# Kernel tuning notes

Measured on AMD Instinct MI355X. Metric: run time of the kernel, lower is better.

## Reference

```python
import jax, jax.numpy as jnp
import numpy as np

E = 16   # n_experts
K = 4    # top_k
NEG = jnp.float32(-1e20)


def _swiglu(x, w1, w2, w3):
    # bias-free SwiGLU expert: (swish(x@w1) * (x@w2)) @ w3
    a = x @ w1
    return (a * jax.nn.sigmoid(a) * (x @ w2)) @ w3


def setup_inputs() -> dict:
    key = jax.random.key(0)
    ks = jax.random.split(key, 9)
    B, S, D, H = 32, 512, 512, 1365  # H = D*2*4//3
    s = 0.02  # weight init scale to keep activations sane
    return {
        "x": jax.random.normal(ks[0], (B, S, D), jnp.float32),
        "gate_w": jax.random.normal(ks[1], (D, E), jnp.float32) * s,
        "routing_bias": jnp.zeros((E,), jnp.float32),
        "w1": jax.random.normal(ks[2], (E, D, H), jnp.float32) * s,
        "w2": jax.random.normal(ks[3], (E, D, H), jnp.float32) * s,
        "w3": jax.random.normal(ks[4], (E, H, D), jnp.float32) * s,
        "sw1": jax.random.normal(ks[5], (D, H), jnp.float32) * s,
        "sw2": jax.random.normal(ks[6], (D, H), jnp.float32) * s,
        "sw3": jax.random.normal(ks[7], (H, D), jnp.float32) * s,
    }


def reference(x, gate_w, routing_bias, w1, w2, w3, sw1, sw2, sw3):
    # gate logits + aux-free load-balancing bias  [B,S,E]
    gate_out = x @ gate_w + routing_bias
    top_v, top_i = jax.lax.top_k(gate_out, K)
    # chosen[b,s,e] = 1 if expert e is in the top-k for token (b,s)
    chosen = jax.nn.one_hot(top_i, E, dtype=x.dtype).sum(axis=-2)
    # scatter top-k values onto a -1e20 background, then softmax over experts
    masked = jnp.where(chosen > 0, gate_out, NEG)
    probs = jax.nn.softmax(masked, axis=-1)
    weights = probs * chosen  # zero outside the chosen set (matches torch mask)
    # shared expert runs on all tokens
    out = _swiglu(x, sw1, sw2, sw3)
    # per-expert SwiGLU, weighted-combined (loop over fixed small E)
    for e in range(E):
        out = out + _swiglu(x, w1[e], w2[e], w3[e]) * weights[..., e:e + 1]
    return out
```

## Files before the change

### kernel.cpp

```cpp
#include <hip/hip_runtime.h>

#define NT    16384
#define DDIM  512
#define HDIM  1365
#define HPAD  1408
#define NEXP  16
#define BK    64
#define BM    128
#define MAXTILES 656
#define MAXSLOTS 83968

typedef unsigned short u16;
typedef unsigned int   u32;
typedef __attribute__((ext_vector_type(8))) __bf16 bf16x8;
typedef __attribute__((ext_vector_type(4))) float  f32x4;
typedef __attribute__((address_space(3))) void lds_void;
typedef __attribute__((address_space(1))) void glb_void;

__device__ __forceinline__ u16 f2bf(float f) {
  union { float f; u32 u; } v; v.f = f;
  u32 u = v.u;
  u += 0x7fffu + ((u >> 16) & 1u);
  return (u16)(u >> 16);
}

__device__ __forceinline__ float bf2f(u16 b) {
  union { u32 u; float f; } v; v.u = ((u32)b) << 16;
  return v.f;
}

__device__ __forceinline__ f32x4 mfma16(bf16x8 a, bf16x8 b, f32x4 c) {
  return __builtin_amdgcn_mfma_f32_16x16x32_bf16(a, b, c, 0, 0, 0);
}

__device__ __forceinline__ void gload16(const u16* g, u16* l) {
  __builtin_amdgcn_global_load_lds((const glb_void*)g, (lds_void*)l, 16, 0, 0);
}

__device__ __forceinline__ bf16x8 lds_frag(const u16* base, int row, int e0) {
  int b = ((row << 7) + (e0 << 1)) ^ ((row & 7) << 4);
  return *(const bf16x8*)((const char*)base + b);
}

__device__ __forceinline__ int swz_n(int bid, int n) {
  int q = n >> 3, r = n & 7;
  int xcd = bid & 7, j = bid >> 3;
  return (xcd < r ? xcd * (q + 1) : r * (q + 1) + (xcd - r) * q) + j;
}

__global__ void convert_x_kernel(const float* __restrict__ in, u16* __restrict__ out, int n8) {
  int i = blockIdx.x * 256 + threadIdx.x;
  if (i >= n8) return;
  float4 a = ((const float4*)in)[2 * i];
  float4 b = ((const float4*)in)[2 * i + 1];
  u16 r[8] = {f2bf(a.x), f2bf(a.y), f2bf(a.z), f2bf(a.w),
              f2bf(b.x), f2bf(b.y), f2bf(b.z), f2bf(b.w)};
  ((uint4*)out)[i] = *(const uint4*)r;
}

__global__ void transpose12_kernel(const float* __restrict__ in, u16* __restrict__ out) {
  __shared__ float tile[32][33];
  int e = blockIdx.z;
  int h0 = blockIdx.x * 32, d0 = blockIdx.y * 32;
  int tx = threadIdx.x, ty = threadIdx.y;
#pragma unroll
  for (int r = 0; r < 4; ++r) {
    int d = d0 + ty + r * 8, h = h0 + tx;
    float v = (h < HDIM) ? in[((size_t)e * DDIM + d) * HDIM + h] : 0.f;
    tile[ty + r * 8][tx] = v;
  }
  __syncthreads();
#pragma unroll
  for (int r = 0; r < 4; ++r) {
    int h = h0 + ty + r * 8, d = d0 + tx;
    out[((size_t)e * HPAD + h) * DDIM + d] = f2bf(tile[tx][ty + r * 8]);
  }
}

__global__ void transpose3_kernel(const float* __restrict__ in, u16* __restrict__ out) {
  __shared__ float tile[32][33];
  int e = blockIdx.z;
  int d0 = blockIdx.x * 32, h0 = blockIdx.y * 32;
  int tx = threadIdx.x, ty = threadIdx.y;
#pragma unroll
  for (int r = 0; r < 4; ++r) {
    int h = h0 + ty + r * 8, d = d0 + tx;
    float v = (h < HDIM) ? in[((size_t)e * HDIM + h) * DDIM + d] : 0.f;
    tile[ty + r * 8][tx] = v;
  }
  __syncthreads();
#pragma unroll
  for (int r = 0; r < 4; ++r) {
    int d = d0 + ty + r * 8, h = h0 + tx;
    out[((size_t)e * DDIM + d) * HPAD + h] = f2bf(tile[tx][ty + r * 8]);
  }
}

__global__ __launch_bounds__(512) void routing_kernel(
    const float* __restrict__ x, const float* __restrict__ gw,
    const float* __restrict__ rbias,
    int* __restrict__ top_e, float* __restrict__ top_w) {
  __shared__ float gwT[NEXP * DDIM];
  int tid = threadIdx.x;
  for (int i = tid; i < NEXP * DDIM; i += 512) {
    int d = i >> 4, e = i & 15;
    gwT[e * DDIM + d] = gw[i];
  }
  __syncthreads();
  int w = tid >> 6, lane = tid & 63;
  int t = blockIdx.x * 8 + w;
  const float* xr = x + (size_t)t * DDIM;
  float xv[8];
#pragma unroll
  for (int k = 0; k < 8; ++k) xv[k] = xr[lane + (k << 6)];
  float acc[NEXP];
#pragma unroll
  for (int e = 0; e < NEXP; ++e) {
    const float* ge = gwT + e * DDIM + lane;
    float s = 0.f;
#pragma unroll
    for (int k = 0; k < 8; ++k) s += xv[k] * ge[k << 6];
#pragma unroll
    for (int off = 32; off; off >>= 1) s += __shfl_xor(s, off);
    acc[e] = s + rbias[e];
  }
  if (lane == 0) {
    int sel[4]; float sv[4];
    unsigned used = 0;
#pragma unroll
    for (int i = 0; i < 4; ++i) {
      float best = -1e30f; int bi = 0;
#pragma unroll
      for (int e = 0; e < NEXP; ++e) {
        bool ok = !((used >> e) & 1u) && acc[e] > best;
        best = ok ? acc[e] : best;
        bi   = ok ? e : bi;
      }
      used |= 1u << bi; sel[i] = bi; sv[i] = best;
    }
    float m = sv[0];
    float ex[4]; float s = 0.f;
#pragma unroll
    for (int i = 0; i < 4; ++i) { ex[i] = __expf(sv[i] - m); s += ex[i]; }
    float inv = 1.f / s;
#pragma unroll
    for (int i = 0; i < 4; ++i) {
      top_e[t * 4 + i] = sel[i];
      top_w[t * 4 + i] = ex[i] * inv;
    }
  }
}

__global__ __launch_bounds__(1024) void rank_kernel(const int* __restrict__ top_e,
                                                    int* __restrict__ counts,
                                                    int* __restrict__ top_pos) {
  __shared__ int hist[NEXP], base[NEXP];
  int tid = threadIdx.x;
  int t = blockIdx.x * 1024 + tid;
  if (tid < NEXP) hist[tid] = 0;
  __syncthreads();
  int e4[4], r4[4];
#pragma unroll
  for (int i = 0; i < 4; ++i) {
    e4[i] = top_e[t * 4 + i];
    r4[i] = atomicAdd(&hist[e4[i]], 1);
  }
  __syncthreads();
  if (tid < NEXP) base[tid] = atomicAdd(&counts[tid], hist[tid]);
  __syncthreads();
#pragma unroll
  for (int i = 0; i < 4; ++i) top_pos[t * 4 + i] = base[e4[i]] + r4[i];
}

__global__ void finalize_kernel(const int* __restrict__ counts, int* __restrict__ slot_off,
                                int* __restrict__ ntiles, int2* __restrict__ desc) {
  if (threadIdx.x != 0) return;
  int off = 0, td = 0;
  for (int e = 0; e < 17; ++e) {
    int c = (e == 16) ? NT : counts[e];
    slot_off[e] = off;
    int nt = (c + BM - 1) / BM;
    for (int i = 0; i < nt; ++i) { desc[td] = make_int2(e, off + i * BM); ++td; }
    off += nt * BM;
  }
  slot_off[17] = off;
  *ntiles = td;
}

__global__ void scatter_kernel(const int* __restrict__ top_e, const float* __restrict__ top_w,
                               const int* __restrict__ top_pos, const int* __restrict__ slot_off,
                               int* __restrict__ tok_pad, float* __restrict__ w_pad,
                               int* __restrict__ pos_list) {
  int t = blockIdx.x * 256 + threadIdx.x;
  if (t >= NT) return;
#pragma unroll
  for (int i = 0; i < 4; ++i) {
    int e = top_e[t * 4 + i];
    int slot = slot_off[e] + top_pos[t * 4 + i];
    tok_pad[slot] = t;
    w_pad[slot] = top_w[t * 4 + i];
    pos_list[t * 4 + i] = slot;
  }
  int sh = slot_off[16] + t;
  tok_pad[sh] = t;
  w_pad[sh] = 1.f;
}

__global__ __launch_bounds__(256, 3) void gemm1_kernel(
    const u16* __restrict__ x_bf, const u16* __restrict__ w1t, const u16* __restrict__ w2t,
    const u16* __restrict__ sw1t, const u16* __restrict__ sw2t,
    const int* __restrict__ ntiles, const int2* __restrict__ desc,
    const int* __restrict__ tok_pad, u16* __restrict__ h, int lo, int ntc) {
  int ti = (lo >> 7) + swz_n(blockIdx.x, ntc);
  if (ti >= *ntiles) return;
  int2 de = desc[ti];
  int e = de.x, m0 = de.y;
  int n0 = blockIdx.y * 64;
  const u16* W1 = (e == 16) ? sw1t : (w1t + (size_t)e * HPAD * DDIM);
  const u16* W2 = (e == 16) ? sw2t : (w2t + (size_t)e * HPAD * DDIM);

  __shared__ u16 xs[BM * BK];
  __shared__ u16 bs[BM * BK];

  int tid = threadIdx.x, w = tid >> 6, lane = tid & 63;
  int wm = w >> 1, wn = w & 1, lr = lane & 15, lk = lane >> 4;

  const u16* ags[4]; const u16* bgs[4];
  int ce = (((lane & 7) ^ ((lane >> 3) & 7)) << 3);
#pragma unroll
  for (int p = 0; p < 4; ++p) {
    int r = w * 32 + p * 8 + (lane >> 3);
    ags[p] = x_bf + (size_t)tok_pad[m0 + r] * DDIM + ce;
    int grp = (w * 32 + p * 8) >> 4;
    const u16* Wsrc = (grp & 1) ? W2 : W1;
    int hrow = n0 + ((grp >> 1) << 4) + (r & 15);
    bgs[p] = Wsrc + (size_t)hrow * DDIM + ce;
  }

  f32x4 acc[4][4] = {};

  for (int ks = 0; ks < DDIM / BK; ++ks) {
    int k0 = ks * BK;
#pragma unroll
    for (int p = 0; p < 4; ++p) {
      gload16(ags[p] + k0, xs + ((w * 32 + p * 8) << 6));
      gload16(bgs[p] + k0, bs + ((w * 32 + p * 8) << 6));
    }
    __syncthreads();
#pragma unroll
    for (int kf = 0; kf < 2; ++kf) {
      int e0 = kf * 32 + lk * 8;
      bf16x8 bfr[4];
#pragma unroll
      for (int nf = 0; nf < 4; ++nf)
        bfr[nf] = lds_frag(bs, wn * 64 + nf * 16 + lr, e0);
#pragma unroll
      for (int mf = 0; mf < 4; ++mf) {
        bf16x8 a = lds_frag(xs, wm * 64 + mf * 16 + lr, e0);
#pragma unroll
        for (int nf = 0; nf < 4; ++nf)
          acc[mf][nf] = mfma16(a, bfr[nf], acc[mf][nf]);
      }
    }
    __syncthreads();
  }

#pragma unroll
  for (int mf = 0; mf < 4; ++mf)
#pragma unroll
    for (int nf = 0; nf < 4; nf += 2)
#pragma unroll
      for (int j = 0; j < 4; ++j) {
        float g = acc[mf][nf][j], u = acc[mf][nf + 1][j];
        float hv = g * u / (1.f + __expf(-g));
        int row = wm * 64 + mf * 16 + lk * 4 + j;
        int hcol = n0 + wn * 32 + (nf >> 1) * 16 + lr;
        h[(size_t)(m0 - lo + row) * HPAD + hcol] = f2bf(hv);
      }
}

template <bool YMODE>
__global__ __launch_bounds__(256, 3) void gemm2_kernel(
    const u16* __restrict__ h, const u16* __restrict__ w3t, const u16* __restrict__ sw3t,
    const int* __restrict__ ntiles, const int2* __restrict__ desc,
    const int* __restrict__ tok_pad, const float* __restrict__ w_pad,
    u16* __restrict__ y, float* __restrict__ out, int lo, int ntc) {
  int ti = (lo >> 7) + swz_n(blockIdx.x, ntc);
  if (ti >= *ntiles) return;
  int2 de = desc[ti];
  int e = de.x, m0 = de.y;
  int n0 = blockIdx.y * 128;
  const u16* W3 = (e == 16) ? sw3t : (w3t + (size_t)e * DDIM * HPAD);

  __shared__ u16 hs[BM * BK];
  __shared__ u16 ws3[BM * BK];
  __shared__ float swl[BM];

  int tid = threadIdx.x, w = tid >> 6, lane = tid & 63;
  int wm = w >> 1, wn = w & 1, lr = lane & 15, lk = lane >> 4;

  if (tid < BM) swl[tid] = w_pad[m0 + tid];

  const u16* ags[4]; const u16* bgs[4];
  int ce = (((lane & 7) ^ ((lane >> 3) & 7)) << 3);
#pragma unroll
  for (int p = 0; p < 4; ++p) {
    int r = w * 32 + p * 8 + (lane >> 3);
    ags[p] = h + (size_t)(m0 - lo + r) * HPAD + ce;
    bgs[p] = W3 + (size_t)(n0 + r) * HPAD + ce;
  }

  f32x4 acc[4][4] = {};

  for (int ks = 0; ks < HPAD / BK; ++ks) {
    int k0 = ks * BK;
#pragma unroll
    for (int p = 0; p < 4; ++p) {
      gload16(ags[p] + k0, hs + ((w * 32 + p * 8) << 6));
      gload16(bgs[p] + k0, ws3 + ((w * 32 + p * 8) << 6));
    }
    __syncthreads();
#pragma unroll
    for (int kf = 0; kf < 2; ++kf) {
      int e0 = kf * 32 + lk * 8;
      bf16x8 bfr[4];
#pragma unroll
      for (int nf = 0; nf < 4; ++nf)
        bfr[nf] = lds_frag(ws3, wn * 64 + nf * 16 + lr, e0);
#pragma unroll
      for (int mf = 0; mf < 4; ++mf) {
        bf16x8 a = lds_frag(hs, wm * 64 + mf * 16 + lr, e0);
#pragma unroll
        for (int nf = 0; nf < 4; ++nf)
          acc[mf][nf] = mfma16(a, bfr[nf], acc[mf][nf]);
      }
    }
    __syncthreads();
  }

#pragma unroll
  for (int mf = 0; mf < 4; ++mf)
#pragma unroll
    for (int j = 0; j < 4; ++j) {
      int row = wm * 64 + mf * 16 + lk * 4 + j;
      float wv = swl[row];
      if constexpr (YMODE) {
        u16* yrow = y + (size_t)(m0 + row) * DDIM + n0;
#pragma unroll
        for (int nf = 0; nf < 4; ++nf)
          yrow[wn * 64 + nf * 16 + lr] = f2bf(acc[mf][nf][j] * wv);
      } else {
        float* orow = out + (size_t)tok_pad[m0 + row] * DDIM + n0;
#pragma unroll
        for (int nf = 0; nf < 4; ++nf)
          atomicAdd(&orow[wn * 64 + nf * 16 + lr], acc[mf][nf][j] * wv);
      }
    }
}

__global__ void reduce_kernel(const u16* __restrict__ y, const int* __restrict__ pos_list,
                              const int* __restrict__ slot_off, float* __restrict__ out) {
  int t = blockIdx.x;
  int c = threadIdx.x;
  int4 pl = ((const int4*)pos_list)[t];
  int sh = slot_off[16] + t;
  ushort4 a = ((const ushort4*)(y + (size_t)sh * DDIM))[c];
  ushort4 b = ((const ushort4*)(y + (size_t)pl.x * DDIM))[c];
  ushort4 d = ((const ushort4*)(y + (size_t)pl.y * DDIM))[c];
  ushort4 e = ((const ushort4*)(y + (size_t)pl.z * DDIM))[c];
  ushort4 f = ((const ushort4*)(y + (size_t)pl.w * DDIM))[c];
  float4 s;
  s.x = bf2f(a.x) + bf2f(b.x) + bf2f(d.x) + bf2f(e.x) + bf2f(f.x);
  s.y = bf2f(a.y) + bf2f(b.y) + bf2f(d.y) + bf2f(e.y) + bf2f(f.y);
  s.z = bf2f(a.z) + bf2f(b.z) + bf2f(d.z) + bf2f(e.z) + bf2f(f.z);
  s.w = bf2f(a.w) + bf2f(b.w) + bf2f(d.w) + bf2f(e.w) + bf2f(f.w);
  ((float4*)(out + (size_t)t * DDIM))[c] = s;
}

extern "C" void kernel_launch(void* const* d_in, const int* in_sizes, int n_in,
                              void* d_out, int out_size, void* d_ws, size_t ws_size,
                              hipStream_t stream) {
  const float* x      = (const float*)d_in[0];
  const float* gate_w = (const float*)d_in[1];
  const float* rbias  = (const float*)d_in[2];
  const float* w1     = (const float*)d_in[3];
  const float* w2     = (const float*)d_in[4];
  const float* w3     = (const float*)d_in[5];
  const float* sw1    = (const float*)d_in[6];
  const float* sw2    = (const float*)d_in[7];
  const float* sw3    = (const float*)d_in[8];
  float* out = (float*)d_out;

  char* ws = (char*)d_ws;
  size_t off = 0;
  auto alloc = [&](size_t bytes) -> char* {
    char* p = ws + off;
    off += (bytes + 255) & ~(size_t)255;
    return p;
  };
  u16* x_bf  = (u16*)alloc((size_t)NT * DDIM * 2);
  u16* w1t   = (u16*)alloc((size_t)NEXP * HPAD * DDIM * 2);
  u16* w2t   = (u16*)alloc((size_t)NEXP * HPAD * DDIM * 2);
  u16* w3t   = (u16*)alloc((size_t)NEXP * DDIM * HPAD * 2);
  u16* sw1t  = (u16*)alloc((size_t)HPAD * DDIM * 2);
  u16* sw2t  = (u16*)alloc((size_t)HPAD * DDIM * 2);
  u16* sw3t  = (u16*)alloc((size_t)DDIM * HPAD * 2);
  int*   counts   = (int*)alloc(64 * 4);
  int*   top_e    = (int*)alloc((size_t)NT * 4 * 4);
  float* top_w    = (float*)alloc((size_t)NT * 4 * 4);
  int*   top_pos  = (int*)alloc((size_t)NT * 4 * 4);
  int*   slot_off = (int*)alloc(32 * 4);
  int*   ntiles   = (int*)alloc(256);
  int2*  desc     = (int2*)alloc((size_t)MAXTILES * 8);
  int*   tok_pad  = (int*)alloc((size_t)MAXSLOTS * 4);
  float* w_pad    = (float*)alloc((size_t)MAXSLOTS * 4);
  int*   pos_list = (int*)alloc((size_t)NT * 4 * 4);
  size_t y_off = off;
  u16* y = (u16*)alloc((size_t)MAXSLOTS * DDIM * 2);
  size_t h_off_y = off;
  (void)in_sizes; (void)n_in; (void)ws_size;

  const size_t per_row = (size_t)HPAD * 2;
  bool ymode;
  size_t h_off, rows_avail;
  size_t avail_y = (ws_size > h_off_y) ? (ws_size - h_off_y) : 0;
  if (avail_y / per_row >= 10496) {
    ymode = true; h_off = h_off_y; rows_avail = avail_y / per_row;
  } else {
    ymode = false; h_off = y_off;
    size_t avail_a = (ws_size > y_off) ? (ws_size - y_off) : 0;
    rows_avail = avail_a / per_row;
  }
  int CS;
  if (rows_avail >= (size_t)MAXSLOTS) CS = MAXSLOTS;
  else CS = (int)((rows_avail / BM) * BM);
  if (CS < BM) CS = BM;
  int NCH = (MAXSLOTS + CS - 1) / CS;
  u16* h = (u16*)(ws + h_off);

  hipMemsetAsync(counts, 0, 64 * 4, stream);
  hipMemsetAsync(tok_pad, 0, (size_t)MAXSLOTS * 4, stream);
  hipMemsetAsync(w_pad, 0, (size_t)MAXSLOTS * 4, stream);
  if (!ymode) hipMemsetAsync(out, 0, (size_t)out_size * 4, stream);

  int n8 = NT * DDIM / 8;
  convert_x_kernel<<<n8 / 256, 256, 0, stream>>>(x, x_bf, n8);

  dim3 tb(32, 8);
  transpose12_kernel<<<dim3(HPAD / 32, DDIM / 32, NEXP), tb, 0, stream>>>(w1, w1t);
  transpose12_kernel<<<dim3(HPAD / 32, DDIM / 32, NEXP), tb, 0, stream>>>(w2, w2t);
  transpose12_kernel<<<dim3(HPAD / 32, DDIM / 32, 1),    tb, 0, stream>>>(sw1, sw1t);
  transpose12_kernel<<<dim3(HPAD / 32, DDIM / 32, 1),    tb, 0, stream>>>(sw2, sw2t);
  transpose3_kernel<<<dim3(DDIM / 32, HPAD / 32, NEXP),  tb, 0, stream>>>(w3, w3t);
  transpose3_kernel<<<dim3(DDIM / 32, HPAD / 32, 1),     tb, 0, stream>>>(sw3, sw3t);

  routing_kernel<<<NT / 8, 512, 0, stream>>>(x, gate_w, rbias, top_e, top_w);
  rank_kernel<<<NT / 1024, 1024, 0, stream>>>(top_e, counts, top_pos);
  finalize_kernel<<<1, 64, 0, stream>>>(counts, slot_off, ntiles, desc);
  scatter_kernel<<<NT / 256, 256, 0, stream>>>(top_e, top_w, top_pos, slot_off,
                                               tok_pad, w_pad, pos_list);

  for (int c = 0; c < NCH; ++c) {
    int lo = c * CS;
    int ntc = (MAXSLOTS - lo < CS ? MAXSLOTS - lo : CS) >> 7;
    gemm1_kernel<<<dim3(ntc, HPAD / 64), 256, 0, stream>>>(
        x_bf, w1t, w2t, sw1t, sw2t, ntiles, desc, tok_pad, h, lo, ntc);
    if (ymode)
      gemm2_kernel<true><<<dim3(ntc, DDIM / 128), 256, 0, stream>>>(
          h, w3t, sw3t, ntiles, desc, tok_pad, w_pad, y, out, lo, ntc);
    else
      gemm2_kernel<false><<<dim3(ntc, DDIM / 128), 256, 0, stream>>>(
          h, w3t, sw3t, ntiles, desc, tok_pad, w_pad, y, out, lo, ntc);
  }
  if (ymode) reduce_kernel<<<NT, 128, 0, stream>>>(y, pos_list, slot_off, out);
}
```

Measured before the change: 672.8 us.

## Enlarge GEMM tiles to 256x256 with double-buffered LDS pipelining

Both grouped GEMMs move from 128-row tiles with 4 waves to 256-row tiles with 8 waves per block. The K loop is now double-buffered, issuing global-to-LDS loads for the next K tile while MFMAs run on the current one, using vmcnt waits, raw barriers and setprio. The LDS layout and swizzle are changed to a split-K-half scheme. The goal is more reuse per byte loaded and hiding load latency, at the cost of more padding per expert, more LDS and registers, and fewer blocks per CU.

New measurement: 658.3 us, median of 2. 1.02x faster.

```diff
diff --git a/kernel.cpp b/kernel.cpp
--- a/kernel.cpp
+++ b/kernel.cpp
@@ -6,9 +6,9 @@
 #define HPAD  1408
 #define NEXP  16
 #define BK    64
-#define BM    128
-#define MAXTILES 656
-#define MAXSLOTS 83968
+#define BM    256
+#define MAXTILES 336
+#define MAXSLOTS 86016
 
 typedef unsigned short u16;
 typedef unsigned int   u32;
@@ -37,9 +37,9 @@
   __builtin_amdgcn_global_load_lds((const glb_void*)g, (lds_void*)l, 16, 0, 0);
 }
 
-__device__ __forceinline__ bf16x8 lds_frag(const u16* base, int row, int e0) {
-  int b = ((row << 7) + (e0 << 1)) ^ ((row & 7) << 4);
-  return *(const bf16x8*)((const char*)base + b);
+__device__ __forceinline__ bf16x8 fragk(const u16* half, int row, int lk) {
+  int b = ((row >> 1) << 7) + (((((row & 1) << 2) | lk) ^ ((row >> 1) & 7)) << 4);
+  return *(const bf16x8*)((const char*)half + b);
 }
 
 __device__ __forceinline__ int swz_n(int bid, int n) {
@@ -206,143 +206,246 @@
   w_pad[sh] = 1.f;
 }
 
-__global__ __launch_bounds__(256, 3) void gemm1_kernel(
+__global__ __launch_bounds__(512, 2) void gemm1_kernel(
     const u16* __restrict__ x_bf, const u16* __restrict__ w1t, const u16* __restrict__ w2t,
     const u16* __restrict__ sw1t, const u16* __restrict__ sw2t,
     const int* __restrict__ ntiles, const int2* __restrict__ desc,
     const int* __restrict__ tok_pad, u16* __restrict__ h, int lo, int ntc) {
-  int ti = (lo >> 7) + swz_n(blockIdx.x, ntc);
+  int ti = (lo >> 8) + swz_n(blockIdx.x, ntc);
   if (ti >= *ntiles) return;
   int2 de = desc[ti];
   int e = de.x, m0 = de.y;
-  int n0 = blockIdx.y * 64;
+  int n0h = blockIdx.y * 128;
   const u16* W1 = (e == 16) ? sw1t : (w1t + (size_t)e * HPAD * DDIM);
   const u16* W2 = (e == 16) ? sw2t : (w2t + (size_t)e * HPAD * DDIM);
 
-  __shared__ u16 xs[BM * BK];
-  __shared__ u16 bs[BM * BK];
+  __shared__ u16 As[32768];
+  __shared__ u16 Bs[32768];
 
   int tid = threadIdx.x, w = tid >> 6, lane = tid & 63;
-  int wm = w >> 1, wn = w & 1, lr = lane & 15, lk = lane >> 4;
-
-  const u16* ags[4]; const u16* bgs[4];
-  int ce = (((lane & 7) ^ ((lane >> 3) & 7)) << 3);
-#pragma unroll
-  for (int p = 0; p < 4; ++p) {
-    int r = w * 32 + p * 8 + (lane >> 3);
-    ags[p] = x_bf + (size_t)tok_pad[m0 + r] * DDIM + ce;
-    int grp = (w * 32 + p * 8) >> 4;
+  int wm = w >> 2, wn = w & 3, lr = lane & 15, lk = lane >> 4;
+
+  int ldsrow0 = tid >> 3, slot = tid & 7;
+  int sx = slot ^ (ldsrow0 & 7);
+  int r0 = ldsrow0 * 2 + (sx >> 2);
+  int sch = (sx & 3) << 3;
+  const u16* a0 = x_bf + (size_t)tok_pad[m0 + r0] * DDIM + sch;
+  const u16* a1 = x_bf + (size_t)tok_pad[m0 + 128 + r0] * DDIM + sch;
+  auto browp = [&](int r) {
+    int grp = r >> 4;
     const u16* Wsrc = (grp & 1) ? W2 : W1;
-    int hrow = n0 + ((grp >> 1) << 4) + (r & 15);
-    bgs[p] = Wsrc + (size_t)hrow * DDIM + ce;
-  }
-
-  f32x4 acc[4][4] = {};
-
-  for (int ks = 0; ks < DDIM / BK; ++ks) {
-    int k0 = ks * BK;
-#pragma unroll
-    for (int p = 0; p < 4; ++p) {
-      gload16(ags[p] + k0, xs + ((w * 32 + p * 8) << 6));
-      gload16(bgs[p] + k0, bs + ((w * 32 + p * 8) << 6));
-    }
-    __syncthreads();
-#pragma unroll
-    for (int kf = 0; kf < 2; ++kf) {
-      int e0 = kf * 32 + lk * 8;
-      bf16x8 bfr[4];
-#pragma unroll
-      for (int nf = 0; nf < 4; ++nf)
-        bfr[nf] = lds_frag(bs, wn * 64 + nf * 16 + lr, e0);
-#pragma unroll
-      for (int mf = 0; mf < 4; ++mf) {
-        bf16x8 a = lds_frag(xs, wm * 64 + mf * 16 + lr, e0);
-#pragma unroll
-        for (int nf = 0; nf < 4; ++nf)
-          acc[mf][nf] = mfma16(a, bfr[nf], acc[mf][nf]);
-      }
-    }
-    __syncthreads();
-  }
-
-#pragma unroll
-  for (int mf = 0; mf < 4; ++mf)
-#pragma unroll
-    for (int nf = 0; nf < 4; nf += 2)
+    int hrow = n0h + ((grp >> 1) << 4) + (r & 15);
+    return Wsrc + (size_t)hrow * DDIM + sch;
+  };
+  const u16* b0 = browp(r0);
+  const u16* b1 = browp(128 + r0);
+  int sdst = w << 9;
+
+  auto stageA = [&](int kc, int kf, int buf) {
+    u16* d = As + buf * 16384 + kf * 8192 + sdst;
+    gload16(a0 + kc + kf * 32, d);
+    gload16(a1 + kc + kf * 32, d + 4096);
+  };
+  auto stageB = [&](int kc, int kf, int buf) {
+    u16* d = Bs + buf * 16384 + kf * 8192 + sdst;
+    gload16(b0 + kc + kf * 32, d);
+    gload16(b1 + kc + kf * 32, d + 4096);
+  };
+
+  f32x4 acc[8][4] = {};
+
+  stageA(0, 0, 0); stageB(0, 0, 0); stageA(0, 1, 0); stageB(0, 1, 0);
+
+  const int NTK = DDIM / BK;
+  for (int t = 0; t < NTK; ++t) {
+    int cur = t & 1, nxt = cur ^ 1;
+    int tn = (t + 1 < NTK) ? t + 1 : t;
+    int kc = tn * BK;
+    const u16* A0 = As + cur * 16384;
+    const u16* A1 = A0 + 8192;
+    const u16* B0 = Bs + cur * 16384;
+    const u16* B1 = B0 + 8192;
+    bf16x8 afr[4], bfr[4];
+    asm volatile("s_waitcnt vmcnt(4)" ::: "memory");
+    __builtin_amdgcn_s_barrier();
+    __builtin_amdgcn_sched_barrier(0);
+    stageA(kc, 0, nxt);
+#pragma unroll
+    for (int nf = 0; nf < 4; ++nf) bfr[nf] = fragk(B0, wn * 64 + nf * 16 + lr, lk);
+#pragma unroll
+    for (int mf = 0; mf < 4; ++mf) afr[mf] = fragk(A0, wm * 128 + mf * 16 + lr, lk);
+    __builtin_amdgcn_s_setprio(1);
+#pragma unroll
+    for (int mf = 0; mf < 4; ++mf)
+#pragma unroll
+      for (int nf = 0; nf < 4; ++nf)
+        acc[mf][nf] = mfma16(afr[mf], bfr[nf], acc[mf][nf]);
+    __builtin_amdgcn_s_setprio(0);
+    stageB(kc, 0, nxt);
+#pragma unroll
+    for (int mf = 0; mf < 4; ++mf) afr[mf] = fragk(A0, wm * 128 + (mf + 4) * 16 + lr, lk);
+    __builtin_amdgcn_s_setprio(1);
+#pragma unroll
+    for (int mf = 0; mf < 4; ++mf)
+#pragma unroll
+      for (int nf = 0; nf < 4; ++nf)
+        acc[mf + 4][nf] = mfma16(afr[mf], bfr[nf], acc[mf + 4][nf]);
+    __builtin_amdgcn_s_setprio(0);
+    asm volatile("s_waitcnt vmcnt(4)" ::: "memory");
+    __builtin_amdgcn_s_barrier();
+    __builtin_amdgcn_sched_barrier(0);
+    stageA(kc, 1, nxt);
+#pragma unroll
+    for (int nf = 0; nf < 4; ++nf) bfr[nf] = fragk(B1, wn * 64 + nf * 16 + lr, lk);
+#pragma unroll
+    for (int mf = 0; mf < 4; ++mf) afr[mf] = fragk(A1, wm * 128 + mf * 16 + lr, lk);
+    __builtin_amdgcn_s_setprio(1);
+#pragma unroll
+    for (int mf = 0; mf < 4; ++mf)
+#pragma unroll
+      for (int nf = 0; nf < 4; ++nf)
+        acc[mf][nf] = mfma16(afr[mf], bfr[nf], acc[mf][nf]);
+    __builtin_amdgcn_s_setprio(0);
+    stageB(kc, 1, nxt);
+#pragma unroll
+    for (int mf = 0; mf < 4; ++mf) afr[mf] = fragk(A1, wm * 128 + (mf + 4) * 16 + lr, lk);
+    __builtin_amdgcn_s_setprio(1);
+#pragma unroll
+    for (int mf = 0; mf < 4; ++mf)
+#pragma unroll
+      for (int nf = 0; nf < 4; ++nf)
+        acc[mf + 4][nf] = mfma16(afr[mf], bfr[nf], acc[mf + 4][nf]);
+    __builtin_amdgcn_s_setprio(0);
+  }
+
+#pragma unroll
+  for (int mf = 0; mf < 8; ++mf)
+#pragma unroll
+    for (int hc = 0; hc < 2; ++hc)
 #pragma unroll
       for (int j = 0; j < 4; ++j) {
-        float g = acc[mf][nf][j], u = acc[mf][nf + 1][j];
+        float g = acc[mf][hc * 2][j], u = acc[mf][hc * 2 + 1][j];
         float hv = g * u / (1.f + __expf(-g));
-        int row = wm * 64 + mf * 16 + lk * 4 + j;
-        int hcol = n0 + wn * 32 + (nf >> 1) * 16 + lr;
+        int row = wm * 128 + mf * 16 + lk * 4 + j;
+        int hcol = n0h + (wn * 2 + hc) * 16 + lr;
         h[(size_t)(m0 - lo + row) * HPAD + hcol] = f2bf(hv);
       }
 }
 
 template <bool YMODE>
-__global__ __launch_bounds__(256, 3) void gemm2_kernel(
+__global__ __launch_bounds__(512, 2) void gemm2_kernel(
     const u16* __restrict__ h, const u16* __restrict__ w3t, const u16* __restrict__ sw3t,
     const int* __restrict__ ntiles, const int2* __restrict__ desc,
     const int* __restrict__ tok_pad, const float* __restrict__ w_pad,
     u16* __restrict__ y, float* __restrict__ out, int lo, int ntc) {
-  int ti = (lo >> 7) + swz_n(blockIdx.x, ntc);
+  int ti = (lo >> 8) + swz_n(blockIdx.x, ntc);
   if (ti >= *ntiles) return;
   int2 de = desc[ti];
   int e = de.x, m0 = de.y;
-  int n0 = blockIdx.y * 128;
+  int n0 = blockIdx.y * 256;
   const u16* W3 = (e == 16) ? sw3t : (w3t + (size_t)e * DDIM * HPAD);
 
-  __shared__ u16 hs[BM * BK];
-  __shared__ u16 ws3[BM * BK];
+  __shared__ u16 As[32768];
+  __shared__ u16 Bs[32768];
   __shared__ float swl[BM];
 
   int tid = threadIdx.x, w = tid >> 6, lane = tid & 63;
-  int wm = w >> 1, wn = w & 1, lr = lane & 15, lk = lane >> 4;
+  int wm = w >> 2, wn = w & 3, lr = lane & 15, lk = lane >> 4;
 
   if (tid < BM) swl[tid] = w_pad[m0 + tid];
 
-  const u16* ags[4]; const u16* bgs[4];
-  int ce = (((lane & 7) ^ ((lane >> 3) & 7)) << 3);
-#pragma unroll
-  for (int p = 0; p < 4; ++p) {
-    int r = w * 32 + p * 8 + (lane >> 3);
-    ags[p] = h + (size_t)(m0 - lo + r) * HPAD + ce;
-    bgs[p] = W3 + (size_t)(n0 + r) * HPAD + ce;
-  }
-
-  f32x4 acc[4][4] = {};
-
-  for (int ks = 0; ks < HPAD / BK; ++ks) {
-    int k0 = ks * BK;
-#pragma unroll
-    for (int p = 0; p < 4; ++p) {
-      gload16(ags[p] + k0, hs + ((w * 32 + p * 8) << 6));
-      gload16(bgs[p] + k0, ws3 + ((w * 32 + p * 8) << 6));
-    }
-    __syncthreads();
-#pragma unroll
-    for (int kf = 0; kf < 2; ++kf) {
-      int e0 = kf * 32 + lk * 8;
-      bf16x8 bfr[4];
-#pragma unroll
-      for (int nf = 0; nf < 4; ++nf)
-        bfr[nf] = lds_frag(ws3, wn * 64 + nf * 16 + lr, e0);
-#pragma unroll
-      for (int mf = 0; mf < 4; ++mf) {
-        bf16x8 a = lds_frag(hs, wm * 64 + mf * 16 + lr, e0);
-#pragma unroll
-        for (int nf = 0; nf < 4; ++nf)
-          acc[mf][nf] = mfma16(a, bfr[nf], acc[mf][nf]);
-      }
-    }
-    __syncthreads();
-  }
-
-#pragma unroll
-  for (int mf = 0; mf < 4; ++mf)
+  int ldsrow0 = tid >> 3, slot = tid & 7;
+  int sx = slot ^ (ldsrow0 & 7);
+  int r0 = ldsrow0 * 2 + (sx >> 2);
+  int sch = (sx & 3) << 3;
+  const u16* a0 = h + (size_t)(m0 - lo + r0) * HPAD + sch;
+  const u16* a1 = a0 + (size_t)128 * HPAD;
+  const u16* b0 = W3 + (size_t)(n0 + r0) * HPAD + sch;
+  const u16* b1 = b0 + (size_t)128 * HPAD;
+  int sdst = w << 9;
+
+  auto stageA = [&](int kc, int kf, int buf) {
+    u16* d = As + buf * 16384 + kf * 8192 + sdst;
+    gload16(a0 + kc + kf * 32, d);
+    gload16(a1 + kc + kf * 32, d + 4096);
+  };
+  auto stageB = [&](int kc, int kf, int buf) {
+    u16* d = Bs + buf * 16384 + kf * 8192 + sdst;
+    gload16(b0 + kc + kf * 32, d);
+    gload16(b1 + kc + kf * 32, d + 4096);
+  };
+
+  f32x4 acc[8][4] = {};
+
+  stageA(0, 0, 0); stageB(0, 0, 0); stageA(0, 1, 0); stageB(0, 1, 0);
+
+  const int NTK = HPAD / BK;
+  for (int t = 0; t < NTK; ++t) {
+    int cur = t & 1, nxt = cur ^ 1;
+    int tn = (t + 1 < NTK) ? t + 1 : t;
+    int kc = tn * BK;
+    const u16* A0 = As + cur * 16384;
+    const u16* A1 = A0 + 8192;
+    const u16* B0 = Bs + cur * 16384;
+    const u16* B1 = B0 + 8192;
+    bf16x8 afr[4], bfr[4];
+    asm volatile("s_waitcnt vmcnt(4)" ::: "memory");
+    __builtin_amdgcn_s_barrier();
+    __builtin_amdgcn_sched_barrier(0);
+    stageA(kc, 0, nxt);
+#pragma unroll
+    for (int nf = 0; nf < 4; ++nf) bfr[nf] = fragk(B0, wn * 64 + nf * 16 + lr, lk);
+#pragma unroll
+    for (int mf = 0; mf < 4; ++mf) afr[mf] = fragk(A0, wm * 128 + mf * 16 + lr, lk);
+    __builtin_amdgcn_s_setprio(1);
+#pragma unroll
+    for (int mf = 0; mf < 4; ++mf)
+#pragma unroll
+      for (int nf = 0; nf < 4; ++nf)
+        acc[mf][nf] = mfma16(afr[mf], bfr[nf], acc[mf][nf]);
+    __builtin_amdgcn_s_setprio(0);
+    stageB(kc, 0, nxt);
+#pragma unroll
+    for (int mf = 0; mf < 4; ++mf) afr[mf] = fragk(A0, wm * 128 + (mf + 4) * 16 + lr, lk);
+    __builtin_amdgcn_s_setprio(1);
+#pragma unroll
+    for (int mf = 0; mf < 4; ++mf)
+#pragma unroll
+      for (int nf = 0; nf < 4; ++nf)
+        acc[mf + 4][nf] = mfma16(afr[mf], bfr[nf], acc[mf + 4][nf]);
+    __builtin_amdgcn_s_setprio(0);
+    asm volatile("s_waitcnt vmcnt(4)" ::: "memory");
+    __builtin_amdgcn_s_barrier();
+    __builtin_amdgcn_sched_barrier(0);
+    stageA(kc, 1, nxt);
+#pragma unroll
+    for (int nf = 0; nf < 4; ++nf) bfr[nf] = fragk(B1, wn * 64 + nf * 16 + lr, lk);
+#pragma unroll
+    for (int mf = 0; mf < 4; ++mf) afr[mf] = fragk(A1, wm * 128 + mf * 16 + lr, lk);
+    __builtin_amdgcn_s_setprio(1);
+#pragma unroll
+    for (int mf = 0; mf < 4; ++mf)
+#pragma unroll
+      for (int nf = 0; nf < 4; ++nf)
+        acc[mf][nf] = mfma16(afr[mf], bfr[nf], acc[mf][nf]);
+    __builtin_amdgcn_s_setprio(0);
+    stageB(kc, 1, nxt);
+#pragma unroll
+    for (int mf = 0; mf < 4; ++mf) afr[mf] = fragk(A1, wm * 128 + (mf + 4) * 16 + lr, lk);
+    __builtin_amdgcn_s_setprio(1);
+#pragma unroll
+    for (int mf = 0; mf < 4; ++mf)
+#pragma unroll
+      for (int nf = 0; nf < 4; ++nf)
+        acc[mf + 4][nf] = mfma16(afr[mf], bfr[nf], acc[mf + 4][nf]);
+    __builtin_amdgcn_s_setprio(0);
+  }
+
+#pragma unroll
+  for (int mf = 0; mf < 8; ++mf)
 #pragma unroll
     for (int j = 0; j < 4; ++j) {
-      int row = wm * 64 + mf * 16 + lk * 4 + j;
+      int row = wm * 128 + mf * 16 + lk * 4 + j;
       float wv = swl[row];
       if constexpr (YMODE) {
         u16* yrow = y + (size_t)(m0 + row) * DDIM + n0;
@@ -424,7 +527,7 @@
   bool ymode;
   size_t h_off, rows_avail;
   size_t avail_y = (ws_size > h_off_y) ? (ws_size - h_off_y) : 0;
-  if (avail_y / per_row >= 10496) {
+  if (avail_y / per_row >= 10752) {
     ymode = true; h_off = h_off_y; rows_avail = avail_y / per_row;
   } else {
     ymode = false; h_off = y_off;
@@ -462,14 +565,14 @@
 
   for (int c = 0; c < NCH; ++c) {
     int lo = c * CS;
-    int ntc = (MAXSLOTS - lo < CS ? MAXSLOTS - lo : CS) >> 7;
-    gemm1_kernel<<<dim3(ntc, HPAD / 64), 256, 0, stream>>>(
+    int ntc = (MAXSLOTS - lo < CS ? MAXSLOTS - lo : CS) >> 8;
+    gemm1_kernel<<<dim3(ntc, HPAD / 128), 512, 0, stream>>>(
         x_bf, w1t, w2t, sw1t, sw2t, ntiles, desc, tok_pad, h, lo, ntc);
     if (ymode)
-      gemm2_kernel<true><<<dim3(ntc, DDIM / 128), 256, 0, stream>>>(
+      gemm2_kernel<true><<<dim3(ntc, DDIM / 256), 512, 0, stream>>>(
           h, w3t, sw3t, ntiles, desc, tok_pad, w_pad, y, out, lo, ntc);
     else
-      gemm2_kernel<false><<<dim3(ntc, DDIM / 128), 256, 0, stream>>>(
+      gemm2_kernel<false><<<dim3(ntc, DDIM / 256), 512, 0, stream>>>(
           h, w3t, sw3t, ntiles, desc, tok_pad, w_pad, y, out, lo, ntc);
   }
   if (ymode) reduce_kernel<<<NT, 128, 0, stream>>>(y, pos_list, slot_off, out);
```
